# Optimization experiments

Measured on AMD Instinct MI355X. Metric: run time of the kernel, lower is better.

## Reference

```python
import jax, jax.numpy as jnp
import numpy as np

# Grid spacing (CartesianGrid3D.dx / .dy)
DX = 1000.0
DY = 1000.0
WENO_EPS = 1e-6  # classic Jiang-Shu smoothness regularizer

NZ, NY, NX = 32, 1024, 1024


def _weno5_recon(qm2, qm1, q0, qp1, qp2):
    """Classic WENO5 (Jiang-Shu) reconstruction of q at the i+1/2 face,
    left-biased (stencil centered on cell i)."""
    c1312 = 13.0 / 12.0
    b0 = c1312 * (qm2 - 2.0 * qm1 + q0) ** 2 + 0.25 * (qm2 - 4.0 * qm1 + 3.0 * q0) ** 2
    b1 = c1312 * (qm1 - 2.0 * q0 + qp1) ** 2 + 0.25 * (qm1 - qp1) ** 2
    b2 = c1312 * (q0 - 2.0 * qp1 + qp2) ** 2 + 0.25 * (3.0 * q0 - 4.0 * qp1 + qp2) ** 2
    a0 = 0.1 / (WENO_EPS + b0) ** 2
    a1 = 0.6 / (WENO_EPS + b1) ** 2
    a2 = 0.3 / (WENO_EPS + b2) ** 2
    p0 = (2.0 * qm2 - 7.0 * qm1 + 11.0 * q0) / 6.0
    p1 = (-qm1 + 5.0 * q0 + 2.0 * qp1) / 6.0
    p2 = (2.0 * q0 + 5.0 * qp1 - qp2) / 6.0
    return (a0 * p0 + a1 * p1 + a2 * p2) / (a0 + a1 + a2)


def _weno5_flux(q, vel, axis):
    """Upwinded WENO5 flux vel * q_face at face i+1/2 along `axis`.
    Edge-padded so the flux array has the same shape as q (faithful to
    recon.weno5_x / weno5_y producing full-shape flux arrays whose interior
    is consumed by the divergence)."""
    q = jnp.moveaxis(q, axis, -1)
    vel = jnp.moveaxis(vel, axis, -1)
    n = q.shape[-1]
    pad = [(0, 0)] * (q.ndim - 1) + [(2, 3)]
    qp = jnp.pad(q, pad, mode='edge')
    sl = lambda o: qp[..., o:o + n]
    qm2, qm1, q0, qp1, qp2, qp3 = sl(0), sl(1), sl(2), sl(3), sl(4), sl(5)
    q_left = _weno5_recon(qm2, qm1, q0, qp1, qp2)          # upwind for vel >= 0
    q_right = _weno5_recon(qp3, qp2, qp1, q0, qm1)         # mirrored, vel < 0
    f = vel * jnp.where(vel >= 0.0, q_left, q_right)
    return jnp.moveaxis(f, -1, axis)


def setup_inputs() -> dict:
    key = jax.random.key(0)
    kh, ku, kv = jax.random.split(key, 3)
    h = jax.random.normal(kh, (NZ, NY, NX), dtype=jnp.float32)
    u = jax.random.normal(ku, (NZ, NY, NX), dtype=jnp.float32)
    v = jax.random.normal(kv, (NZ, NY, NX), dtype=jnp.float32)
    return {"h": h, "u": u, "v": v}


def reference(h, u, v):
    # fe: flux through east face (x), fn: flux through north face (y)
    fe = _weno5_flux(h, u, axis=2)
    fn = _weno5_flux(h, v, axis=1)
    div = ((fe[1:-1, 2:-2, 2:-2] - fe[1:-1, 2:-2, 1:-3]) / DX
           + (fn[1:-1, 2:-2, 2:-2] - fn[1:-1, 1:-3, 2:-2]) / DY)
    out = jnp.zeros_like(h)
    out = out.at[1:-1, 2:-2, 2:-2].set(-div)
    return out
```

## Files before the change

### kernel.cpp

```cpp
#include <hip/hip_runtime.h>

#define NZ 32
#define NY 1024
#define NX 1024

__device__ __forceinline__ float rcpf(float x) { return __builtin_amdgcn_rcpf(x); }

__device__ __forceinline__ float weno5(float qm2, float qm1, float q0, float qp1, float qp2) {
    const float c1312 = 13.0f / 12.0f;
    float t0 = qm2 - 2.0f * qm1 + q0;
    float u0 = qm2 - 4.0f * qm1 + 3.0f * q0;
    float b0 = c1312 * t0 * t0 + 0.25f * u0 * u0;
    float t1 = qm1 - 2.0f * q0 + qp1;
    float u1 = qm1 - qp1;
    float b1 = c1312 * t1 * t1 + 0.25f * u1 * u1;
    float t2 = q0 - 2.0f * qp1 + qp2;
    float u2 = 3.0f * q0 - 4.0f * qp1 + qp2;
    float b2 = c1312 * t2 * t2 + 0.25f * u2 * u2;
    float e0 = 1e-6f + b0;
    float e1 = 1e-6f + b1;
    float e2 = 1e-6f + b2;
    float a0 = 0.1f * rcpf(e0 * e0);
    float a1 = 0.6f * rcpf(e1 * e1);
    float a2 = 0.3f * rcpf(e2 * e2);
    const float c16 = 1.0f / 6.0f;
    float p0 = (2.0f * qm2 - 7.0f * qm1 + 11.0f * q0) * c16;
    float p1 = (-qm1 + 5.0f * q0 + 2.0f * qp1) * c16;
    float p2 = (2.0f * q0 + 5.0f * qp1 - qp2) * c16;
    return (a0 * p0 + a1 * p1 + a2 * p2) * rcpf(a0 + a1 + a2);
}

__device__ __forceinline__ float upwind_flux(float vel, float qm2, float qm1, float q0,
                                             float qp1, float qp2, float qp3) {
    bool up = vel >= 0.0f;
    float s0 = up ? qm2 : qp3;
    float s1 = up ? qm1 : qp2;
    float s2 = up ? q0  : qp1;
    float s3 = up ? qp1 : q0;
    float s4 = up ? qp2 : qm1;
    return vel * weno5(s0, s1, s2, s3, s4);
}

__global__ __launch_bounds__(256) void adv_kernel(const float* __restrict__ h,
                                                  const float* __restrict__ u,
                                                  const float* __restrict__ v,
                                                  float* __restrict__ out) {
    int x = blockIdx.x * blockDim.x + threadIdx.x;
    int y = blockIdx.y;
    int z = blockIdx.z;
    size_t base = ((size_t)z * NY + y) * NX;
    size_t idx = base + x;

    bool interior = (z >= 1) && (z <= NZ - 2) && (y >= 2) && (y <= NY - 3) &&
                    (x >= 2) && (x <= NX - 3);
    if (!interior) {
        out[idx] = 0.0f;
        return;
    }

    const float* row = h + base;
    float hx[7];
#pragma unroll
    for (int k = 0; k < 7; ++k) {
        int xx = x - 3 + k;
        xx = xx < 0 ? 0 : (xx > NX - 1 ? NX - 1 : xx);
        hx[k] = row[xx];
    }
    float fe_hi = upwind_flux(u[idx],     hx[1], hx[2], hx[3], hx[4], hx[5], hx[6]);
    float fe_lo = upwind_flux(u[idx - 1], hx[0], hx[1], hx[2], hx[3], hx[4], hx[5]);

    float hy[7];
#pragma unroll
    for (int k = 0; k < 7; ++k) {
        int yy = y - 3 + k;
        yy = yy < 0 ? 0 : (yy > NY - 1 ? NY - 1 : yy);
        hy[k] = h[((size_t)z * NY + yy) * NX + x];
    }
    float fn_hi = upwind_flux(v[idx],      hy[1], hy[2], hy[3], hy[4], hy[5], hy[6]);
    float fn_lo = upwind_flux(v[idx - NX], hy[0], hy[1], hy[2], hy[3], hy[4], hy[5]);

    const float inv_dx = 1.0f / 1000.0f;
    const float inv_dy = 1.0f / 1000.0f;
    out[idx] = -((fe_hi - fe_lo) * inv_dx + (fn_hi - fn_lo) * inv_dy);
}

extern "C" void kernel_launch(void* const* d_in, const int* in_sizes, int n_in,
                              void* d_out, int out_size, void* d_ws, size_t ws_size,
                              hipStream_t stream) {
    const float* h = (const float*)d_in[0];
    const float* u = (const float*)d_in[1];
    const float* v = (const float*)d_in[2];
    float* out = (float*)d_out;

    dim3 block(256, 1, 1);
    dim3 grid(NX / 256, NY, NZ);
    adv_kernel<<<grid, block, 0, stream>>>(h, u, v, out);
}
```

Before: 450.4 us.

## March threads along y with register sliding window and shuffle-shared x fluxes

Each thread now walks 16 rows in y, keeping a 7-point register window of h and reusing the previous row's north flux as the lower face, which halves the y-direction WENO work. The west-face x flux is taken from the neighbouring lane via a shuffle, so only lane 0 of each wavefront recomputes it. The WENO weights are also rewritten to drop the three reciprocals by cross-multiplying the squared smoothness terms. Together these cut redundant flux evaluations and loads, at the cost of fewer blocks in the grid. The cross-multiplication can overflow or underflow float for large or very small smoothness values.

```diff
diff --git a/kernel.cpp b/kernel.cpp
--- a/kernel.cpp
+++ b/kernel.cpp
@@ -3,6 +3,7 @@
 #define NZ 32
 #define NY 1024
 #define NX 1024
+#define TY 16
 
 __device__ __forceinline__ float rcpf(float x) { return __builtin_amdgcn_rcpf(x); }
 
@@ -20,9 +21,10 @@
     float e0 = 1e-6f + b0;
     float e1 = 1e-6f + b1;
     float e2 = 1e-6f + b2;
-    float a0 = 0.1f * rcpf(e0 * e0);
-    float a1 = 0.6f * rcpf(e1 * e1);
-    float a2 = 0.3f * rcpf(e2 * e2);
+    float s0 = e0 * e0, s1 = e1 * e1, s2 = e2 * e2;
+    float a0 = 0.1f * (s1 * s2);
+    float a1 = 0.6f * (s0 * s2);
+    float a2 = 0.3f * (s0 * s1);
     const float c16 = 1.0f / 6.0f;
     float p0 = (2.0f * qm2 - 7.0f * qm1 + 11.0f * q0) * c16;
     float p1 = (-qm1 + 5.0f * q0 + 2.0f * qp1) * c16;
@@ -45,43 +47,78 @@
                                                   const float* __restrict__ u,
                                                   const float* __restrict__ v,
                                                   float* __restrict__ out) {
-    int x = blockIdx.x * blockDim.x + threadIdx.x;
-    int y = blockIdx.y;
-    int z = blockIdx.z;
-    size_t base = ((size_t)z * NY + y) * NX;
-    size_t idx = base + x;
+    const int tid = threadIdx.x;
+    const int x  = blockIdx.x * 256 + tid;
+    const int z  = blockIdx.z;
+    const int y0 = blockIdx.y * TY;
+    const size_t zoff = (size_t)z * (NY * NX);
+    const float* __restrict__ hz = h + zoff;
+    const float* __restrict__ uz = u + zoff;
+    const float* __restrict__ vz = v + zoff;
+    float* __restrict__ oz = out + zoff;
 
-    bool interior = (z >= 1) && (z <= NZ - 2) && (y >= 2) && (y <= NY - 3) &&
-                    (x >= 2) && (x <= NX - 3);
-    if (!interior) {
-        out[idx] = 0.0f;
+    if (z == 0 || z == NZ - 1) {
+#pragma unroll
+        for (int t = 0; t < TY; ++t) oz[(y0 + t) * NX + x] = 0.0f;
         return;
     }
 
-    const float* row = h + base;
-    float hx[7];
+    int xc[7];
 #pragma unroll
     for (int k = 0; k < 7; ++k) {
         int xx = x - 3 + k;
-        xx = xx < 0 ? 0 : (xx > NX - 1 ? NX - 1 : xx);
-        hx[k] = row[xx];
+        xc[k] = xx < 0 ? 0 : (xx > NX - 1 ? NX - 1 : xx);
     }
-    float fe_hi = upwind_flux(u[idx],     hx[1], hx[2], hx[3], hx[4], hx[5], hx[6]);
-    float fe_lo = upwind_flux(u[idx - 1], hx[0], hx[1], hx[2], hx[3], hx[4], hx[5]);
+    const int xm1 = (x > 0) ? x - 1 : 0;
+    const bool xin = (x >= 2) && (x <= NX - 3);
+    const bool lane0 = (tid & 63) == 0;
 
     float hy[7];
 #pragma unroll
     for (int k = 0; k < 7; ++k) {
-        int yy = y - 3 + k;
+        int yy = y0 - 3 + k;
         yy = yy < 0 ? 0 : (yy > NY - 1 ? NY - 1 : yy);
-        hy[k] = h[((size_t)z * NY + yy) * NX + x];
+        hy[k] = hz[yy * NX + x];
     }
-    float fn_hi = upwind_flux(v[idx],      hy[1], hy[2], hy[3], hy[4], hy[5], hy[6]);
-    float fn_lo = upwind_flux(v[idx - NX], hy[0], hy[1], hy[2], hy[3], hy[4], hy[5]);
 
-    const float inv_dx = 1.0f / 1000.0f;
-    const float inv_dy = 1.0f / 1000.0f;
-    out[idx] = -((fe_hi - fe_lo) * inv_dx + (fn_hi - fn_lo) * inv_dy);
+    {
+    }
+    const int ym1 = (y0 > 0) ? y0 - 1 : 0;
+    float fn_lo = upwind_flux(vz[ym1 * NX + x], hy[0], hy[1], hy[2], hy[3], hy[4], hy[5]);
+
+#pragma unroll
+    for (int t = 0; t < TY; ++t) {
+        const int y = y0 + t;
+        const int row = y * NX;
+
+        float hx0 = hz[row + xc[0]];
+        float hx1 = hz[row + xc[1]];
+        float hx2 = hz[row + xc[2]];
+        float hx3 = hy[3];
+        float hx4 = hz[row + xc[4]];
+        float hx5 = hz[row + xc[5]];
+        float hx6 = hz[row + xc[6]];
+
+        float fe_hi = upwind_flux(uz[row + x], hx1, hx2, hx3, hx4, hx5, hx6);
+        float fe_lo = __shfl_up(fe_hi, 1);
+        if (lane0) {
+            fe_lo = upwind_flux(uz[row + xm1], hx0, hx1, hx2, hx3, hx4, hx5);
+        }
+
+        float fn_hi = upwind_flux(vz[row + x], hy[1], hy[2], hy[3], hy[4], hy[5], hy[6]);
+
+        const float inv_d = 1.0f / 1000.0f;
+        float val = -((fe_hi - fe_lo) + (fn_hi - fn_lo)) * inv_d;
+        bool interior = xin && (y >= 2) && (y <= NY - 3);
+        oz[row + x] = interior ? val : 0.0f;
+
+        fn_lo = fn_hi;
+#pragma unroll
+        for (int k = 0; k < 6; ++k) hy[k] = hy[k + 1];
+        int yn = y + 4;
+        yn = yn > NY - 1 ? NY - 1 : yn;
+        hy[6] = hz[yn * NX + x];
+    }
 }
 
 extern "C" void kernel_launch(void* const* d_in, const int* in_sizes, int n_in,
@@ -93,6 +130,6 @@
     float* out = (float*)d_out;
 
     dim3 block(256, 1, 1);
-    dim3 grid(NX / 256, NY, NZ);
+    dim3 grid(NX / 256, NY / TY, NZ);
     adv_kernel<<<grid, block, 0, stream>>>(h, u, v, out);
 }
```

After: 440.5 us. 1.02x faster.
